# Kernel tuning notes

Hardware: AMD Instinct MI355X
Metric: run time of the kernel (lower is better)

The kernel has to match this reference:

```python
import jax, jax.numpy as jnp
import numpy as np

N_NODES = 100000


def mean_aggregate(features, src, dst, n_nodes):
    # copy_u: gather source features per edge -> [E, d]
    msgs = features[src]
    # mean reduce by destination node (segment mean)
    summed = jax.ops.segment_sum(msgs, dst, num_segments=n_nodes)
    deg = jax.ops.segment_sum(jnp.ones((src.shape[0],), features.dtype), dst,
                              num_segments=n_nodes)
    return summed / jnp.maximum(deg, 1.0)[:, None]


def setup_inputs() -> dict:
    key = jax.random.key(0)
    k1, k2, k3 = jax.random.split(key, 3)
    features = jax.random.normal(k1, (N_NODES, 64), dtype=jnp.float32)
    src = jax.random.randint(k2, (1600000,), 0, N_NODES, dtype=jnp.int64)
    dst = jax.random.randint(k3, (1600000,), 0, N_NODES, dtype=jnp.int64)
    return {"features": features, "src": src, "dst": dst}


def reference(features, src, dst):
    n = features.shape[0]
    x = mean_aggregate(features, src, dst, n)   # gcn1
    x2 = mean_aggregate(x, src, dst, n)         # gcn2
    # stack([x, x2], dim=1).mean(dim=1) == elementwise average
    return (x + x2) * 0.5
```

## Files before the change

### kernel.cpp

```cpp
#include <hip/hip_runtime.h>


#define BNODES   128
#define MAXBUCK  1024
#define CBLOCKS  512
#define CONVB    1024
#define CTHREADS 256
#define CAP      8192

typedef float v4f __attribute__((ext_vector_type(4)));
typedef unsigned int v4u __attribute__((ext_vector_type(4)));
typedef unsigned short v4h __attribute__((ext_vector_type(4)));

__device__ __forceinline__ unsigned short benc(float f) {
    union { float f; unsigned u; } x;
    x.f = f;
    unsigned u = x.u;
    return (unsigned short)((u + 0x7FFFu + ((u >> 16) & 1u)) >> 16);
}
__device__ __forceinline__ float f_lo(unsigned u) {
    union { unsigned u; float f; } x; x.u = u << 16; return x.f;
}
__device__ __forceinline__ float f_hi(unsigned u) {
    union { unsigned u; float f; } x; x.u = u & 0xFFFF0000u; return x.f;
}

__global__ void zero_kernel(int* __restrict__ p, int n) {
    for (int i = threadIdx.x; i < n; i += blockDim.x) p[i] = 0;
}

__global__ void prep_kernel(const float* __restrict__ feat,
                            unsigned short* __restrict__ feat_h, int total4,
                            const int* __restrict__ dst, int E, int nbuck,
                            int* __restrict__ gcount, int* __restrict__ blockBase) {
    __shared__ int hist[MAXBUCK];
    if (blockIdx.x < CONVB) {
        int stride = CONVB * blockDim.x;
        for (int t = blockIdx.x * blockDim.x + threadIdx.x; t < total4; t += stride) {
            const float4 v = *reinterpret_cast<const float4*>(feat + (size_t)t * 4);
            v4h h;
            h.x = benc(v.x); h.y = benc(v.y); h.z = benc(v.z); h.w = benc(v.w);
            __builtin_nontemporal_store(h, reinterpret_cast<v4h*>(feat_h + (size_t)t * 4));
        }
        return;
    }
    int cb = blockIdx.x - CONVB;
    for (int i = threadIdx.x; i < nbuck; i += blockDim.x) hist[i] = 0;
    __syncthreads();
    int per = (E + CBLOCKS - 1) / CBLOCKS;
    int beg = cb * per;
    int end = min(E, beg + per);
    for (int e = beg + threadIdx.x; e < end; e += blockDim.x)
        atomicAdd(&hist[dst[e] >> 7], 1);
    __syncthreads();
    for (int i = threadIdx.x; i < nbuck; i += blockDim.x)
        blockBase[(size_t)cb * nbuck + i] = atomicAdd(&gcount[i], hist[i]);
}

__global__ void scan_kernel(const int* __restrict__ gcount, int nbuck,
                            int* __restrict__ bucketOffs) {
    __shared__ int lds[MAXBUCK];
    int tid = threadIdx.x;
    lds[tid] = (tid < nbuck) ? gcount[tid] : 0;
    __syncthreads();
    for (int s = 1; s < MAXBUCK; s <<= 1) {
        int v = (tid >= s) ? lds[tid - s] : 0;
        __syncthreads();
        lds[tid] += v;
        __syncthreads();
    }
    if (tid < nbuck) bucketOffs[tid + 1] = lds[tid];
    if (tid == 0) bucketOffs[0] = 0;
}

__global__ void fill_kernel(const int* __restrict__ src, const int* __restrict__ dst,
                            int E, int nbuck,
                            const int* __restrict__ bucketOffs,
                            const int* __restrict__ blockBase,
                            unsigned int* __restrict__ recs) {
    __shared__ int cur[MAXBUCK];
    for (int i = threadIdx.x; i < nbuck; i += blockDim.x)
        cur[i] = bucketOffs[i] + blockBase[(size_t)blockIdx.x * nbuck + i];
    __syncthreads();
    int per = (E + gridDim.x - 1) / gridDim.x;
    int beg = blockIdx.x * per;
    int end = min(E, beg + per);
    for (int e = beg + threadIdx.x; e < end; e += blockDim.x) {
        int d = dst[e];
        int b = d >> 7;
        int pos = atomicAdd(&cur[b], 1);
        recs[pos] = ((unsigned)src[e] << 7) | (unsigned)(d & 127);
    }
}

__launch_bounds__(512)
__global__ void sortagg_kernel(const unsigned int* __restrict__ recs,
                               const int* __restrict__ bucketOffs,
                               const unsigned short* __restrict__ feat_h,
                               int nbuck, int N,
                               int* __restrict__ offs,
                               int* __restrict__ edge_src,
                               unsigned short* __restrict__ buf_xh) {
    __shared__ unsigned int list[CAP];
    __shared__ int hist[BNODES], cur[BNODES], offl[BNODES + 1];
    int b = blockIdx.x;
    int tid = threadIdx.x;
    int beg = bucketOffs[b];
    int end = bucketOffs[b + 1];
    int num = min(end - beg, CAP);
    if (tid < BNODES) hist[tid] = 0;
    __syncthreads();
    for (int k = tid; k < num; k += 512)
        atomicAdd(&hist[recs[beg + k] & 127], 1);
    __syncthreads();
    if (tid < BNODES) cur[tid] = hist[tid];
    __syncthreads();
#pragma unroll
    for (int s = 1; s < BNODES; s <<= 1) {
        int v = (tid < BNODES && tid >= s) ? cur[tid - s] : 0;
        __syncthreads();
        if (tid < BNODES) cur[tid] += v;
        __syncthreads();
    }
    int lo = b << 7;
    if (tid < BNODES) {
        int excl = tid ? cur[tid - 1] : 0;
        offl[tid] = excl;
        if (lo + tid < N) offs[lo + tid] = beg + excl;
    }
    if (tid == 0) offl[BNODES] = num;
    if (b == nbuck - 1 && tid == 0) offs[N] = end;
    __syncthreads();
    if (tid < BNODES) cur[tid] = offl[tid];
    __syncthreads();
    for (int k = tid; k < num; k += 512) {
        unsigned rec = recs[beg + k];
        int ld = rec & 127;
        int pos = atomicAdd(&cur[ld], 1);
        list[pos] = rec >> 7;
    }
    __syncthreads();
    for (int k = tid; k < num; k += 512)
        edge_src[beg + k] = (int)list[k];
    int g = tid >> 3;
    int c = tid & 7;
    for (int r = g; r < BNODES; r += 64) {
        int node = lo + r;
        if (node >= N) break;
        int nb = offl[r];
        int ne = offl[r + 1];
        float a[8];
#pragma unroll
        for (int j = 0; j < 8; ++j) a[j] = 0.f;
        int k = nb;
        for (; k + 4 <= ne; k += 4) {
            int s0 = (int)list[k + 0];
            int s1 = (int)list[k + 1];
            int s2 = (int)list[k + 2];
            int s3 = (int)list[k + 3];
            const uint4 u0 = *reinterpret_cast<const uint4*>(feat_h + ((size_t)s0 << 6) + c * 8);
            const uint4 u1 = *reinterpret_cast<const uint4*>(feat_h + ((size_t)s1 << 6) + c * 8);
            const uint4 u2 = *reinterpret_cast<const uint4*>(feat_h + ((size_t)s2 << 6) + c * 8);
            const uint4 u3 = *reinterpret_cast<const uint4*>(feat_h + ((size_t)s3 << 6) + c * 8);
            a[0] += f_lo(u0.x) + f_lo(u1.x) + f_lo(u2.x) + f_lo(u3.x);
            a[1] += f_hi(u0.x) + f_hi(u1.x) + f_hi(u2.x) + f_hi(u3.x);
            a[2] += f_lo(u0.y) + f_lo(u1.y) + f_lo(u2.y) + f_lo(u3.y);
            a[3] += f_hi(u0.y) + f_hi(u1.y) + f_hi(u2.y) + f_hi(u3.y);
            a[4] += f_lo(u0.z) + f_lo(u1.z) + f_lo(u2.z) + f_lo(u3.z);
            a[5] += f_hi(u0.z) + f_hi(u1.z) + f_hi(u2.z) + f_hi(u3.z);
            a[6] += f_lo(u0.w) + f_lo(u1.w) + f_lo(u2.w) + f_lo(u3.w);
            a[7] += f_hi(u0.w) + f_hi(u1.w) + f_hi(u2.w) + f_hi(u3.w);
        }
        for (; k < ne; ++k) {
            int s = (int)list[k];
            const uint4 u = *reinterpret_cast<const uint4*>(feat_h + ((size_t)s << 6) + c * 8);
            a[0] += f_lo(u.x); a[1] += f_hi(u.x);
            a[2] += f_lo(u.y); a[3] += f_hi(u.y);
            a[4] += f_lo(u.z); a[5] += f_hi(u.z);
            a[6] += f_lo(u.w); a[7] += f_hi(u.w);
        }
        float inv = (ne > nb) ? 1.0f / (float)(ne - nb) : 0.0f;
        v4u h;
        h.x = (unsigned)benc(a[0] * inv) | ((unsigned)benc(a[1] * inv) << 16);
        h.y = (unsigned)benc(a[2] * inv) | ((unsigned)benc(a[3] * inv) << 16);
        h.z = (unsigned)benc(a[4] * inv) | ((unsigned)benc(a[5] * inv) << 16);
        h.w = (unsigned)benc(a[6] * inv) | ((unsigned)benc(a[7] * inv) << 16);
        __builtin_nontemporal_store(h, reinterpret_cast<v4u*>(buf_xh + ((size_t)node << 6) + c * 8));
    }
}

__launch_bounds__(256)
__global__ void agg1_kernel(const unsigned short* __restrict__ xin,
                            const int* __restrict__ offs,
                            const int* __restrict__ edge_src,
                            float* __restrict__ outf, int N) {
    int t = blockIdx.x * blockDim.x + threadIdx.x;
    int n = t >> 3;
    int c = t & 7;
    if (n >= N) return;
    int beg = offs[n];
    int end = offs[n + 1];
    float a[8];
#pragma unroll
    for (int j = 0; j < 8; ++j) a[j] = 0.f;
    int k = beg;
    int s[8];
    bool have = (k + 8 <= end);
    if (have) {
#pragma unroll
        for (int i = 0; i < 8; ++i) s[i] = edge_src[k + i];
    }
    while (have) {
        int ns[8];
        bool nhave = (k + 16 <= end);
        if (nhave) {
#pragma unroll
            for (int i = 0; i < 8; ++i) ns[i] = edge_src[k + 8 + i];
        }
#pragma unroll
        for (int i = 0; i < 8; ++i) {
            const uint4 u = *reinterpret_cast<const uint4*>(xin + ((size_t)s[i] << 6) + c * 8);
            a[0] += f_lo(u.x); a[1] += f_hi(u.x);
            a[2] += f_lo(u.y); a[3] += f_hi(u.y);
            a[4] += f_lo(u.z); a[5] += f_hi(u.z);
            a[6] += f_lo(u.w); a[7] += f_hi(u.w);
        }
        k += 8;
        if (nhave) {
#pragma unroll
            for (int i = 0; i < 8; ++i) s[i] = ns[i];
        }
        have = nhave;
    }
    for (; k < end; ++k) {
        int sk = edge_src[k];
        const uint4 u = *reinterpret_cast<const uint4*>(xin + ((size_t)sk << 6) + c * 8);
        a[0] += f_lo(u.x); a[1] += f_hi(u.x);
        a[2] += f_lo(u.y); a[3] += f_hi(u.y);
        a[4] += f_lo(u.z); a[5] += f_hi(u.z);
        a[6] += f_lo(u.w); a[7] += f_hi(u.w);
    }
    float inv = (end > beg) ? 1.0f / (float)(end - beg) : 0.0f;
#pragma unroll
    for (int j = 0; j < 8; ++j) a[j] *= inv;
    const uint4 us = *reinterpret_cast<const uint4*>(xin + ((size_t)n << 6) + c * 8);
    v4f r0, r1;
    r0.x = (f_lo(us.x) + a[0]) * 0.5f;
    r0.y = (f_hi(us.x) + a[1]) * 0.5f;
    r0.z = (f_lo(us.y) + a[2]) * 0.5f;
    r0.w = (f_hi(us.y) + a[3]) * 0.5f;
    r1.x = (f_lo(us.z) + a[4]) * 0.5f;
    r1.y = (f_hi(us.z) + a[5]) * 0.5f;
    r1.z = (f_lo(us.w) + a[6]) * 0.5f;
    r1.w = (f_hi(us.w) + a[7]) * 0.5f;
    float* op = outf + ((size_t)n << 6) + c * 8;
    __builtin_nontemporal_store(r0, reinterpret_cast<v4f*>(op));
    __builtin_nontemporal_store(r1, reinterpret_cast<v4f*>(op + 4));
}

static inline size_t align_up(size_t x, size_t a) { return (x + a - 1) & ~(a - 1); }

extern "C" void kernel_launch(void* const* d_in, const int* in_sizes, int n_in,
                              void* d_out, int out_size, void* d_ws, size_t ws_size,
                              hipStream_t stream) {
    const float* feat = (const float*)d_in[0];
    const int*   src  = (const int*)d_in[1];
    const int*   dst  = (const int*)d_in[2];
    float* out = (float*)d_out;

    const int D = 64;
    int N = in_sizes[0] / D;
    int E = in_sizes[1];
    int nbuck = (N + BNODES - 1) / BNODES;

    char* ws = (char*)d_ws;
    size_t off = 0;
    unsigned short* feat_h = (unsigned short*)(ws + off); off = align_up(off + (size_t)N * D * sizeof(unsigned short), 256);
    unsigned short* buf_xh = (unsigned short*)(ws + off); off = align_up(off + (size_t)N * D * sizeof(unsigned short), 256);
    unsigned int* recs = (unsigned int*)(ws + off); off = align_up(off + (size_t)E * sizeof(unsigned int), 256);
    int* blockBase = (int*)(ws + off);  off = align_up(off + (size_t)CBLOCKS * nbuck * sizeof(int), 256);
    int* gcount    = (int*)(ws + off);  off = align_up(off + (size_t)MAXBUCK * sizeof(int), 256);
    int* bucketOffs= (int*)(ws + off);  off = align_up(off + (size_t)(MAXBUCK + 1) * sizeof(int), 256);
    int* edge_src = (int*)recs;
    int* offs     = blockBase;
    (void)ws_size;

    zero_kernel<<<1, 1024, 0, stream>>>(gcount, MAXBUCK);
    prep_kernel<<<CONVB + CBLOCKS, CTHREADS, 0, stream>>>(feat, feat_h, N * D / 4,
                                                          dst, E, nbuck, gcount, blockBase);
    scan_kernel<<<1, MAXBUCK, 0, stream>>>(gcount, nbuck, bucketOffs);
    fill_kernel<<<CBLOCKS, CTHREADS, 0, stream>>>(src, dst, E, nbuck, bucketOffs, blockBase, recs);
    sortagg_kernel<<<nbuck, 512, 0, stream>>>(recs, bucketOffs, feat_h, nbuck, N,
                                              offs, edge_src, buf_xh);
    int grid_a = (N * 8 + 255) / 256;
    agg1_kernel<<<grid_a, 256, 0, stream>>>(buf_xh, offs, edge_src, out, N);
}
```

Before: 121.0 us.

## Use dynamic row tickets and bucket-tiled LDS edge lists in aggregation kernels

Both aggregation kernels now hand out destination rows to 8-lane groups through a shared atomic ticket counter instead of a fixed stride, to balance uneven per-node degrees within a block. The second-layer kernel is rewritten to process one 128-node bucket per 512-thread block, first staging that bucket's edge source indices into LDS, then gathering from there, mirroring the first layer. The edge_src writeback in sortagg is moved after the gather loop. The cost is extra LDS staging and atomics, and lower occupancy from the 32KB LDS per block in the second kernel.

```diff
diff --git a/kernel.cpp b/kernel.cpp
--- a/kernel.cpp
+++ b/kernel.cpp
@@ -23,6 +23,38 @@
 }
 __device__ __forceinline__ float f_hi(unsigned u) {
     union { unsigned u; float f; } x; x.u = u & 0xFFFF0000u; return x.f;
+}
+
+__device__ __forceinline__ void gather_acc(const unsigned short* __restrict__ xin,
+                                           const unsigned int* list,
+                                           int nb, int ne, int c, float* a) {
+    int k = nb;
+    for (; k + 4 <= ne; k += 4) {
+        int s0 = (int)list[k + 0];
+        int s1 = (int)list[k + 1];
+        int s2 = (int)list[k + 2];
+        int s3 = (int)list[k + 3];
+        const uint4 u0 = *reinterpret_cast<const uint4*>(xin + ((size_t)s0 << 6) + c * 8);
+        const uint4 u1 = *reinterpret_cast<const uint4*>(xin + ((size_t)s1 << 6) + c * 8);
+        const uint4 u2 = *reinterpret_cast<const uint4*>(xin + ((size_t)s2 << 6) + c * 8);
+        const uint4 u3 = *reinterpret_cast<const uint4*>(xin + ((size_t)s3 << 6) + c * 8);
+        a[0] += f_lo(u0.x) + f_lo(u1.x) + f_lo(u2.x) + f_lo(u3.x);
+        a[1] += f_hi(u0.x) + f_hi(u1.x) + f_hi(u2.x) + f_hi(u3.x);
+        a[2] += f_lo(u0.y) + f_lo(u1.y) + f_lo(u2.y) + f_lo(u3.y);
+        a[3] += f_hi(u0.y) + f_hi(u1.y) + f_hi(u2.y) + f_hi(u3.y);
+        a[4] += f_lo(u0.z) + f_lo(u1.z) + f_lo(u2.z) + f_lo(u3.z);
+        a[5] += f_hi(u0.z) + f_hi(u1.z) + f_hi(u2.z) + f_hi(u3.z);
+        a[6] += f_lo(u0.w) + f_lo(u1.w) + f_lo(u2.w) + f_lo(u3.w);
+        a[7] += f_hi(u0.w) + f_hi(u1.w) + f_hi(u2.w) + f_hi(u3.w);
+    }
+    for (; k < ne; ++k) {
+        int s = (int)list[k];
+        const uint4 u = *reinterpret_cast<const uint4*>(xin + ((size_t)s << 6) + c * 8);
+        a[0] += f_lo(u.x); a[1] += f_hi(u.x);
+        a[2] += f_lo(u.y); a[3] += f_hi(u.y);
+        a[4] += f_lo(u.z); a[5] += f_hi(u.z);
+        a[6] += f_lo(u.w); a[7] += f_hi(u.w);
+    }
 }
 
 __global__ void zero_kernel(int* __restrict__ p, int n) {
@@ -103,12 +135,14 @@
                                unsigned short* __restrict__ buf_xh) {
     __shared__ unsigned int list[CAP];
     __shared__ int hist[BNODES], cur[BNODES], offl[BNODES + 1];
+    __shared__ int ticket;
     int b = blockIdx.x;
     int tid = threadIdx.x;
     int beg = bucketOffs[b];
     int end = bucketOffs[b + 1];
     int num = min(end - beg, CAP);
     if (tid < BNODES) hist[tid] = 0;
+    if (tid == 0) ticket = 0;
     __syncthreads();
     for (int k = tid; k < num; k += 512)
         atomicAdd(&hist[recs[beg + k] & 127], 1);
@@ -135,50 +169,24 @@
     __syncthreads();
     for (int k = tid; k < num; k += 512) {
         unsigned rec = recs[beg + k];
-        int ld = rec & 127;
-        int pos = atomicAdd(&cur[ld], 1);
+        int pos = atomicAdd(&cur[rec & 127], 1);
         list[pos] = rec >> 7;
     }
     __syncthreads();
-    for (int k = tid; k < num; k += 512)
-        edge_src[beg + k] = (int)list[k];
-    int g = tid >> 3;
     int c = tid & 7;
-    for (int r = g; r < BNODES; r += 64) {
+    while (true) {
+        int r = 0;
+        if (c == 0) r = atomicAdd(&ticket, 1);
+        r = __shfl(r, 0, 8);
+        if (r >= BNODES) break;
         int node = lo + r;
-        if (node >= N) break;
+        if (node >= N) continue;
         int nb = offl[r];
         int ne = offl[r + 1];
         float a[8];
 #pragma unroll
         for (int j = 0; j < 8; ++j) a[j] = 0.f;
-        int k = nb;
-        for (; k + 4 <= ne; k += 4) {
-            int s0 = (int)list[k + 0];
-            int s1 = (int)list[k + 1];
-            int s2 = (int)list[k + 2];
-            int s3 = (int)list[k + 3];
-            const uint4 u0 = *reinterpret_cast<const uint4*>(feat_h + ((size_t)s0 << 6) + c * 8);
-            const uint4 u1 = *reinterpret_cast<const uint4*>(feat_h + ((size_t)s1 << 6) + c * 8);
-            const uint4 u2 = *reinterpret_cast<const uint4*>(feat_h + ((size_t)s2 << 6) + c * 8);
-            const uint4 u3 = *reinterpret_cast<const uint4*>(feat_h + ((size_t)s3 << 6) + c * 8);
-            a[0] += f_lo(u0.x) + f_lo(u1.x) + f_lo(u2.x) + f_lo(u3.x);
-            a[1] += f_hi(u0.x) + f_hi(u1.x) + f_hi(u2.x) + f_hi(u3.x);
-            a[2] += f_lo(u0.y) + f_lo(u1.y) + f_lo(u2.y) + f_lo(u3.y);
-            a[3] += f_hi(u0.y) + f_hi(u1.y) + f_hi(u2.y) + f_hi(u3.y);
-            a[4] += f_lo(u0.z) + f_lo(u1.z) + f_lo(u2.z) + f_lo(u3.z);
-            a[5] += f_hi(u0.z) + f_hi(u1.z) + f_hi(u2.z) + f_hi(u3.z);
-            a[6] += f_lo(u0.w) + f_lo(u1.w) + f_lo(u2.w) + f_lo(u3.w);
-            a[7] += f_hi(u0.w) + f_hi(u1.w) + f_hi(u2.w) + f_hi(u3.w);
-        }
-        for (; k < ne; ++k) {
-            int s = (int)list[k];
-            const uint4 u = *reinterpret_cast<const uint4*>(feat_h + ((size_t)s << 6) + c * 8);
-            a[0] += f_lo(u.x); a[1] += f_hi(u.x);
-            a[2] += f_lo(u.y); a[3] += f_hi(u.y);
-            a[4] += f_lo(u.z); a[5] += f_hi(u.z);
-            a[6] += f_lo(u.w); a[7] += f_hi(u.w);
-        }
+        gather_acc(feat_h, list, nb, ne, c, a);
         float inv = (ne > nb) ? 1.0f / (float)(ne - nb) : 0.0f;
         v4u h;
         h.x = (unsigned)benc(a[0] * inv) | ((unsigned)benc(a[1] * inv) << 16);
@@ -187,75 +195,61 @@
         h.w = (unsigned)benc(a[6] * inv) | ((unsigned)benc(a[7] * inv) << 16);
         __builtin_nontemporal_store(h, reinterpret_cast<v4u*>(buf_xh + ((size_t)node << 6) + c * 8));
     }
-}
-
-__launch_bounds__(256)
+    for (int k = tid; k < num; k += 512)
+        edge_src[beg + k] = (int)list[k];
+}
+
+__launch_bounds__(512)
 __global__ void agg1_kernel(const unsigned short* __restrict__ xin,
                             const int* __restrict__ offs,
                             const int* __restrict__ edge_src,
                             float* __restrict__ outf, int N) {
-    int t = blockIdx.x * blockDim.x + threadIdx.x;
-    int n = t >> 3;
-    int c = t & 7;
-    if (n >= N) return;
-    int beg = offs[n];
-    int end = offs[n + 1];
-    float a[8];
-#pragma unroll
-    for (int j = 0; j < 8; ++j) a[j] = 0.f;
-    int k = beg;
-    int s[8];
-    bool have = (k + 8 <= end);
-    if (have) {
-#pragma unroll
-        for (int i = 0; i < 8; ++i) s[i] = edge_src[k + i];
-    }
-    while (have) {
-        int ns[8];
-        bool nhave = (k + 16 <= end);
-        if (nhave) {
-#pragma unroll
-            for (int i = 0; i < 8; ++i) ns[i] = edge_src[k + 8 + i];
-        }
-#pragma unroll
-        for (int i = 0; i < 8; ++i) {
-            const uint4 u = *reinterpret_cast<const uint4*>(xin + ((size_t)s[i] << 6) + c * 8);
-            a[0] += f_lo(u.x); a[1] += f_hi(u.x);
-            a[2] += f_lo(u.y); a[3] += f_hi(u.y);
-            a[4] += f_lo(u.z); a[5] += f_hi(u.z);
-            a[6] += f_lo(u.w); a[7] += f_hi(u.w);
-        }
-        k += 8;
-        if (nhave) {
-#pragma unroll
-            for (int i = 0; i < 8; ++i) s[i] = ns[i];
-        }
-        have = nhave;
-    }
-    for (; k < end; ++k) {
-        int sk = edge_src[k];
-        const uint4 u = *reinterpret_cast<const uint4*>(xin + ((size_t)sk << 6) + c * 8);
-        a[0] += f_lo(u.x); a[1] += f_hi(u.x);
-        a[2] += f_lo(u.y); a[3] += f_hi(u.y);
-        a[4] += f_lo(u.z); a[5] += f_hi(u.z);
-        a[6] += f_lo(u.w); a[7] += f_hi(u.w);
-    }
-    float inv = (end > beg) ? 1.0f / (float)(end - beg) : 0.0f;
-#pragma unroll
-    for (int j = 0; j < 8; ++j) a[j] *= inv;
-    const uint4 us = *reinterpret_cast<const uint4*>(xin + ((size_t)n << 6) + c * 8);
-    v4f r0, r1;
-    r0.x = (f_lo(us.x) + a[0]) * 0.5f;
-    r0.y = (f_hi(us.x) + a[1]) * 0.5f;
-    r0.z = (f_lo(us.y) + a[2]) * 0.5f;
-    r0.w = (f_hi(us.y) + a[3]) * 0.5f;
-    r1.x = (f_lo(us.z) + a[4]) * 0.5f;
-    r1.y = (f_hi(us.z) + a[5]) * 0.5f;
-    r1.z = (f_lo(us.w) + a[6]) * 0.5f;
-    r1.w = (f_hi(us.w) + a[7]) * 0.5f;
-    float* op = outf + ((size_t)n << 6) + c * 8;
-    __builtin_nontemporal_store(r0, reinterpret_cast<v4f*>(op));
-    __builtin_nontemporal_store(r1, reinterpret_cast<v4f*>(op + 4));
+    __shared__ unsigned int list[CAP];
+    __shared__ int offl[BNODES + 1];
+    __shared__ int ticket;
+    int b = blockIdx.x;
+    int tid = threadIdx.x;
+    int lo = b << 7;
+    int nrows = min(BNODES, N - lo);
+    int beg = offs[lo];
+    int end = offs[lo + nrows];
+    int num = min(end - beg, CAP);
+    if (tid <= nrows) offl[tid] = offs[lo + tid] - beg;
+    if (tid == 0) ticket = 0;
+    __syncthreads();
+    for (int k = tid; k < num; k += 512)
+        list[k] = (unsigned)edge_src[beg + k];
+    __syncthreads();
+    int c = tid & 7;
+    while (true) {
+        int r = 0;
+        if (c == 0) r = atomicAdd(&ticket, 1);
+        r = __shfl(r, 0, 8);
+        if (r >= nrows) break;
+        int node = lo + r;
+        int nb = offl[r];
+        int ne = offl[r + 1];
+        float a[8];
+#pragma unroll
+        for (int j = 0; j < 8; ++j) a[j] = 0.f;
+        gather_acc(xin, list, nb, ne, c, a);
+        float inv = (ne > nb) ? 1.0f / (float)(ne - nb) : 0.0f;
+#pragma unroll
+        for (int j = 0; j < 8; ++j) a[j] *= inv;
+        const uint4 us = *reinterpret_cast<const uint4*>(xin + ((size_t)node << 6) + c * 8);
+        v4f r0, r1;
+        r0.x = (f_lo(us.x) + a[0]) * 0.5f;
+        r0.y = (f_hi(us.x) + a[1]) * 0.5f;
+        r0.z = (f_lo(us.y) + a[2]) * 0.5f;
+        r0.w = (f_hi(us.y) + a[3]) * 0.5f;
+        r1.x = (f_lo(us.z) + a[4]) * 0.5f;
+        r1.y = (f_hi(us.z) + a[5]) * 0.5f;
+        r1.z = (f_lo(us.w) + a[6]) * 0.5f;
+        r1.w = (f_hi(us.w) + a[7]) * 0.5f;
+        float* op = outf + ((size_t)node << 6) + c * 8;
+        __builtin_nontemporal_store(r0, reinterpret_cast<v4f*>(op));
+        __builtin_nontemporal_store(r1, reinterpret_cast<v4f*>(op + 4));
+    }
 }
 
 static inline size_t align_up(size_t x, size_t a) { return (x + a - 1) & ~(a - 1); }
@@ -292,6 +286,5 @@
     fill_kernel<<<CBLOCKS, CTHREADS, 0, stream>>>(src, dst, E, nbuck, bucketOffs, blockBase, recs);
     sortagg_kernel<<<nbuck, 512, 0, stream>>>(recs, bucketOffs, feat_h, nbuck, N,
                                               offs, edge_src, buf_xh);
-    int grid_a = (N * 8 + 255) / 256;
-    agg1_kernel<<<grid_a, 256, 0, stream>>>(buf_xh, offs, edge_src, out, N);
-}
+    agg1_kernel<<<nbuck, 512, 0, stream>>>(buf_xh, offs, edge_src, out, N);
+}
```

New measurement: 118.2 us. -2.3%, faster.
